# Kernel tuning notes

Measured on AMD Instinct MI355X. Metric: run time of the kernel, lower is better.

## Reference

```python
import jax, jax.numpy as jnp
import numpy as np

N, K, F_IN, T, OUT = 50000, 25, 128, 256, 128
EPS = 1e-3  # TF BatchNormalization default epsilon


def batchnorm_train(x, gamma, beta):
    # training-mode BN: biased batch statistics over axis 0
    mean = jnp.mean(x, axis=0)
    var = jnp.var(x, axis=0)
    return (x - mean) * jax.lax.rsqrt(var + EPS) * gamma + beta


def setup_inputs() -> dict:
    key = jax.random.key(0)
    ks = jax.random.split(key, 6)
    return {
        "self_nodes": jax.random.normal(ks[0], (N, F_IN), dtype=jnp.float32),
        "neigh_nodes": jax.random.normal(ks[1], (N, K, F_IN), dtype=jnp.float32),
        "len_adj_nodes": jax.random.randint(ks[2], (N,), 1, K + 1, dtype=jnp.int32),
        "Wt": jax.random.normal(ks[3], (F_IN, T), dtype=jnp.float32) * 0.05,
        "bt": jnp.zeros((T,), dtype=jnp.float32),
        "g1": jnp.ones((T,), dtype=jnp.float32),
        "b1": jnp.zeros((T,), dtype=jnp.float32),
        "Wn": jax.random.normal(ks[4], (T, OUT), dtype=jnp.float32) * 0.05,
        "Ws": jax.random.normal(ks[5], (F_IN, OUT), dtype=jnp.float32) * 0.05,
        "g2": jnp.ones((2 * OUT,), dtype=jnp.float32),
        "b2": jnp.zeros((2 * OUT,), dtype=jnp.float32),
    }


def reference(self_nodes, neigh_nodes, len_adj_nodes, Wt, bt, g1, b1, Wn, Ws, g2, b2):
    # len_adj_nodes is accepted by the original call() but unused.
    # transform neighbor features: [N, K, F_IN] -> [N, K, T]
    neigh = jnp.einsum('nkf,ft->nkt', neigh_nodes, Wt) + bt
    # bn1 over flattened [N*K, T] (training mode)
    neigh = batchnorm_train(neigh.reshape(-1, T), g1, b1).reshape(N, K, T)
    # pool_op = reduce_max over the neighbor axis
    pooled = jnp.max(neigh, axis=1)            # [N, T]
    neigh_out = pooled @ Wn                     # [N, OUT], no bias
    self_out = self_nodes @ Ws                  # [N, OUT], no bias
    out = jnp.concatenate([self_out, neigh_out], axis=1)  # use_concat=True
    out = batchnorm_train(out, g2, b2)
    return jax.nn.relu(out)
```

## Files before the change

### kernel.cpp

```cpp
#include <hip/hip_runtime.h>


#define NN 50000
#define KN 25
#define FIN 128
#define TD 256
#define OUTD 128
#define BN_EPS 1e-3f
#define NSLOTS 64
#define K1_GRID 512
#define NGROUPS (NN / 2)

typedef float f32x4 __attribute__((ext_vector_type(4)));
typedef short bf16x8 __attribute__((ext_vector_type(8)));

__device__ __forceinline__ ushort f2bf(float f) {
    uint u = __builtin_bit_cast(uint, f);
    return (ushort)((u + 0x7FFFu + ((u >> 16) & 1u)) >> 16);
}
__device__ __forceinline__ uint pk2(float a, float b) {
    return (uint)f2bf(a) | ((uint)f2bf(b) << 16);
}
__device__ __forceinline__ float bflo(uint u) {
    return __builtin_bit_cast(float, u << 16);
}
__device__ __forceinline__ float bfhi(uint u) {
    return __builtin_bit_cast(float, u & 0xffff0000u);
}

__global__ __launch_bounds__(256) void k0_prep(
    const float* __restrict__ Ws, const float* __restrict__ Wn,
    float* __restrict__ stats, ushort* __restrict__ WsT, ushort* __restrict__ WnT)
{
    const int gid = blockIdx.x * 256 + threadIdx.x;
    if (gid < 65536) {
        stats[gid] = 0.f;
    } else if (gid < 81920) {
        const int t = gid - 65536, col = t >> 7, k = t & 127;
        WsT[col * FIN + k] = f2bf(Ws[k * OUTD + col]);
    } else {
        const int t = gid - 81920, col = t >> 8, k = t & 255;
        WnT[col * TD + k] = f2bf(Wn[k * OUTD + col]);
    }
}

__global__ __launch_bounds__(256, 2) void k1_gemm_pool(
    const float* __restrict__ neigh, const float* __restrict__ Wt,
    const float* __restrict__ bt, uint* __restrict__ nmm,
    float* __restrict__ s1sum, float* __restrict__ s1sq)
{
    __shared__ ushort lds[32768];
    const int tid = threadIdx.x;
    const int wave = tid >> 6, lane = tid & 63;
    const int quad = lane >> 4, l16 = lane & 15;
    const int cbase = wave * 64;

    {
        const float4* w4 = (const float4*)Wt;
        #pragma unroll
        for (int i = 0; i < 32; ++i) {
            const int e = tid + i * 256;
            const int k = e >> 6, c4 = (e & 63) << 2;
            const float4 v = w4[e];
            uint* dst = (uint*)&lds[k * 256 + c4];
            dst[0] = pk2(v.x, v.y);
            dst[1] = pk2(v.z, v.w);
        }
    }
    __syncthreads();

    bf16x8 bf[4][4];
    #pragma unroll
    for (int nt = 0; nt < 4; ++nt) {
        const int col = cbase + nt * 16 + l16;
        #pragma unroll
        for (int ks = 0; ks < 4; ++ks) {
            #pragma unroll
            for (int j = 0; j < 8; ++j)
                bf[nt][ks][j] = (short)lds[(ks * 32 + quad * 8 + j) * 256 + col];
        }
    }
    __syncthreads();

    float bv[4];
    #pragma unroll
    for (int n = 0; n < 4; ++n) bv[n] = bt[cbase + n * 16 + l16];

    float S[4] = {0.f, 0.f, 0.f, 0.f}, Q[4] = {0.f, 0.f, 0.f, 0.f};

    int g = blockIdx.x;
    {
        const float4* src = (const float4*)(neigh + (size_t)g * 6400);
        #pragma unroll
        for (int i = 0; i < 7; ++i) {
            const int idx = tid + i * 256;
            if (idx < 1600) {
                const float4 v = src[idx];
                const int r = idx >> 5;
                const int pr = r + (r >= 25 ? 7 : 0);
                uint* dst = (uint*)&lds[pr * 136 + ((idx & 31) << 2)];
                dst[0] = pk2(v.x, v.y);
                dst[1] = pk2(v.z, v.w);
            }
        }
    }
    __syncthreads();

    int cur = 0;
    for (; g < NGROUPS; g += K1_GRID) {
        const int gn = g + K1_GRID;
        float4 pre[7];
        if (gn < NGROUPS) {
            const float4* src = (const float4*)(neigh + (size_t)gn * 6400);
            #pragma unroll
            for (int i = 0; i < 7; ++i) {
                const int idx = tid + i * 256;
                if (idx < 1600) pre[i] = src[idx];
            }
        }
        const ushort* Ab = lds + cur * 8704;
        f32x4 acc[4][4];
        #pragma unroll
        for (int m = 0; m < 4; ++m)
            #pragma unroll
            for (int n = 0; n < 4; ++n)
                acc[m][n] = (f32x4){0.f, 0.f, 0.f, 0.f};
        #pragma unroll
        for (int m = 0; m < 4; ++m) {
            bf16x8 af[4];
            #pragma unroll
            for (int ks = 0; ks < 4; ++ks)
                af[ks] = *(const bf16x8*)&Ab[(m * 16 + l16) * 136 + ks * 32 + quad * 8];
            #pragma unroll
            for (int n = 0; n < 4; ++n)
                #pragma unroll
                for (int ks = 0; ks < 4; ++ks)
                    acc[m][n] = __builtin_amdgcn_mfma_f32_16x16x32_bf16(af[ks], bf[n][ks], acc[m][n], 0, 0, 0);
        }
        #pragma unroll
        for (int gi = 0; gi < 2; ++gi) {
            const int node = g * 2 + gi;
            #pragma unroll
            for (int n = 0; n < 4; ++n) {
                float mx = -3.4e38f, mn = 3.4e38f;
                #pragma unroll
                for (int i = 0; i < 4; ++i) {
                    const float v = acc[2 * gi][n][i] + bv[n];
                    mx = fmaxf(mx, v); mn = fminf(mn, v);
                    S[n] += v; Q[n] = fmaf(v, v, Q[n]);
                }
                #pragma unroll
                for (int i = 0; i < 4; ++i) {
                    if (quad * 4 + i < 9) {
                        const float v = acc[2 * gi + 1][n][i] + bv[n];
                        mx = fmaxf(mx, v); mn = fminf(mn, v);
                        S[n] += v; Q[n] = fmaf(v, v, Q[n]);
                    }
                }
                mx = fmaxf(mx, __shfl_xor(mx, 16)); mx = fmaxf(mx, __shfl_xor(mx, 32));
                mn = fminf(mn, __shfl_xor(mn, 16)); mn = fminf(mn, __shfl_xor(mn, 32));
                if (lane < 16)
                    nmm[node * TD + cbase + n * 16 + lane] = pk2(mx, mn);
            }
        }
        if (gn < NGROUPS) {
            ushort* Aw = lds + (cur ^ 1) * 8704;
            #pragma unroll
            for (int i = 0; i < 7; ++i) {
                const int idx = tid + i * 256;
                if (idx < 1600) {
                    const int r = idx >> 5;
                    const int pr = r + (r >= 25 ? 7 : 0);
                    uint* dst = (uint*)&Aw[pr * 136 + ((idx & 31) << 2)];
                    dst[0] = pk2(pre[i].x, pre[i].y);
                    dst[1] = pk2(pre[i].z, pre[i].w);
                }
            }
        }
        __syncthreads();
        cur ^= 1;
    }
    #pragma unroll
    for (int n = 0; n < 4; ++n) {
        float s = S[n]; s += __shfl_xor(s, 16); s += __shfl_xor(s, 32);
        float q = Q[n]; q += __shfl_xor(q, 16); q += __shfl_xor(q, 32);
        if (lane < 16) {
            const int col = cbase + n * 16 + lane;
            const int slot = blockIdx.x & (NSLOTS - 1);
            atomicAdd(&s1sum[slot * TD + col], s);
            atomicAdd(&s1sq[slot * TD + col], q);
        }
    }
}

__global__ __launch_bounds__(256) void k_stats(
    const float* __restrict__ ssum, const float* __restrict__ ssq,
    const float* __restrict__ g, const float* __restrict__ b,
    float invM, float* __restrict__ a, float* __restrict__ cc)
{
    const int c = threadIdx.x;
    float s = 0.f, q = 0.f;
    for (int j = 0; j < NSLOTS; ++j) { s += ssum[j * TD + c]; q += ssq[j * TD + c]; }
    const float mean = s * invM;
    const float var = q * invM - mean * mean;
    const float A = rsqrtf(var + BN_EPS) * g[c];
    a[c] = A;
    cc[c] = fmaf(-mean, A, b[c]);
}

__global__ __launch_bounds__(256, 2) void k2_gemm2(
    const float* __restrict__ selfn, const uint* __restrict__ nmm,
    const ushort* __restrict__ WsT, const ushort* __restrict__ WnT,
    const float* __restrict__ s1sum, const float* __restrict__ s1sq,
    const float* __restrict__ g1, const float* __restrict__ b1,
    float* __restrict__ Y, float* __restrict__ s2sum, float* __restrict__ s2sq)
{
    __shared__ ushort lds[25600];
    __shared__ float aL[256], cL[256];
    const int tid = threadIdx.x;
    const int wave = tid >> 6, lane = tid & 63;
    const int quad = lane >> 4, l16 = lane & 15;
    const int R0 = blockIdx.x * 64;

    {
        const int c = tid;
        float s = 0.f, q = 0.f;
        #pragma unroll 8
        for (int j = 0; j < NSLOTS; ++j) { s += s1sum[j * TD + c]; q += s1sq[j * TD + c]; }
        const float invM = 1.f / (float)((size_t)NN * KN);
        const float mean = s * invM;
        const float var = q * invM - mean * mean;
        const float A = rsqrtf(var + BN_EPS) * g1[c];
        aL[c] = A;
        cL[c] = fmaf(-mean, A, b1[c]);
    }

    {
        const float4* s4 = (const float4*)selfn;
        #pragma unroll
        for (int i = 0; i < 8; ++i) {
            const int e = tid + i * 256;
            const int r = e >> 5, k4 = e & 31;
            const int gr = R0 + r;
            const float4 v = (gr < NN) ? s4[(size_t)gr * 32 + k4] : make_float4(0.f, 0.f, 0.f, 0.f);
            uint* dst = (uint*)&lds[r * 136 + (k4 << 2)];
            dst[0] = pk2(v.x, v.y);
            dst[1] = pk2(v.z, v.w);
        }
    }
    __syncthreads();

    {
        const uint4* m4 = (const uint4*)nmm;
        #pragma unroll
        for (int i = 0; i < 16; ++i) {
            const int e = tid + i * 256;
            const int r = e >> 6, c4 = e & 63;
            const int gr = R0 + r;
            uint4 v;
            if (gr < NN) v = m4[(size_t)gr * 64 + c4];
            else { v.x = 0u; v.y = 0u; v.z = 0u; v.w = 0u; }
            const float4 a = *(const float4*)&aL[c4 << 2];
            const float4 c = *(const float4*)&cL[c4 << 2];
            const float p0 = (a.x >= 0.f) ? fmaf(a.x, bflo(v.x), c.x) : fmaf(a.x, bfhi(v.x), c.x);
            const float p1 = (a.y >= 0.f) ? fmaf(a.y, bflo(v.y), c.y) : fmaf(a.y, bfhi(v.y), c.y);
            const float p2 = (a.z >= 0.f) ? fmaf(a.z, bflo(v.z), c.z) : fmaf(a.z, bfhi(v.z), c.z);
            const float p3 = (a.w >= 0.f) ? fmaf(a.w, bflo(v.w), c.w) : fmaf(a.w, bfhi(v.w), c.w);
            uint* dst = (uint*)&lds[8704 + r * 264 + (c4 << 2)];
            dst[0] = pk2(p0, p1);
            dst[1] = pk2(p2, p3);
        }
    }
    __syncthreads();

    f32x4 acc[4][4];
    #pragma unroll
    for (int m = 0; m < 4; ++m)
        #pragma unroll
        for (int n = 0; n < 4; ++n)
            acc[m][n] = (f32x4){0.f, 0.f, 0.f, 0.f};

    if (wave < 2) {
        const int cb = wave * 64;
        bf16x8 bfr[4][4];
        #pragma unroll
        for (int nt = 0; nt < 4; ++nt)
            #pragma unroll
            for (int ks = 0; ks < 4; ++ks)
                bfr[nt][ks] = *(const bf16x8*)&WsT[(cb + nt * 16 + l16) * FIN + ks * 32 + quad * 8];
        #pragma unroll
        for (int m = 0; m < 4; ++m) {
            bf16x8 af[4];
            #pragma unroll
            for (int ks = 0; ks < 4; ++ks)
                af[ks] = *(const bf16x8*)&lds[(m * 16 + l16) * 136 + ks * 32 + quad * 8];
            #pragma unroll
            for (int nt = 0; nt < 4; ++nt)
                #pragma unroll
                for (int ks = 0; ks < 4; ++ks)
                    acc[m][nt] = __builtin_amdgcn_mfma_f32_16x16x32_bf16(af[ks], bfr[nt][ks], acc[m][nt], 0, 0, 0);
        }
    } else {
        const int cb = (wave - 2) * 64;
        bf16x8 bfr[4][8];
        #pragma unroll
        for (int nt = 0; nt < 4; ++nt)
            #pragma unroll
            for (int ks = 0; ks < 8; ++ks)
                bfr[nt][ks] = *(const bf16x8*)&WnT[(cb + nt * 16 + l16) * TD + ks * 32 + quad * 8];
        #pragma unroll
        for (int m = 0; m < 4; ++m) {
            bf16x8 af[8];
            #pragma unroll
            for (int ks = 0; ks < 8; ++ks)
                af[ks] = *(const bf16x8*)&lds[8704 + (m * 16 + l16) * 264 + ks * 32 + quad * 8];
            #pragma unroll
            for (int nt = 0; nt < 4; ++nt)
                #pragma unroll
                for (int ks = 0; ks < 8; ++ks)
                    acc[m][nt] = __builtin_amdgcn_mfma_f32_16x16x32_bf16(af[ks], bfr[nt][ks], acc[m][nt], 0, 0, 0);
        }
    }

    const int colb = wave * 64;
    float S[4] = {0.f, 0.f, 0.f, 0.f}, Q[4] = {0.f, 0.f, 0.f, 0.f};
    #pragma unroll
    for (int m = 0; m < 4; ++m) {
        #pragma unroll
        for (int nt = 0; nt < 4; ++nt) {
            #pragma unroll
            for (int i = 0; i < 4; ++i) {
                const int row = R0 + m * 16 + quad * 4 + i;
                const float v = acc[m][nt][i];
                if (row < NN) {
                    Y[(size_t)row * TD + colb + nt * 16 + l16] = v;
                    S[nt] += v;
                    Q[nt] = fmaf(v, v, Q[nt]);
                }
            }
        }
    }
    #pragma unroll
    for (int nt = 0; nt < 4; ++nt) {
        float s = S[nt]; s += __shfl_xor(s, 16); s += __shfl_xor(s, 32);
        float q = Q[nt]; q += __shfl_xor(q, 16); q += __shfl_xor(q, 32);
        if (lane < 16) {
            const int col = colb + nt * 16 + lane;
            const int slot = blockIdx.x & (NSLOTS - 1);
            atomicAdd(&s2sum[slot * TD + col], s);
            atomicAdd(&s2sq[slot * TD + col], q);
        }
    }
}

__global__ __launch_bounds__(256) void k7_bn_relu(
    float* __restrict__ out, const float* __restrict__ a2, const float* __restrict__ c2)
{
    const int idx = blockIdx.x * 256 + threadIdx.x;
    const int c4 = idx & 63;
    float4 y = ((const float4*)out)[idx];
    const float4 a = ((const float4*)a2)[c4];
    const float4 c = ((const float4*)c2)[c4];
    y.x = fmaxf(0.f, fmaf(a.x, y.x, c.x));
    y.y = fmaxf(0.f, fmaf(a.y, y.y, c.y));
    y.z = fmaxf(0.f, fmaf(a.z, y.z, c.z));
    y.w = fmaxf(0.f, fmaf(a.w, y.w, c.w));
    ((float4*)out)[idx] = y;
}

extern "C" void kernel_launch(void* const* d_in, const int* in_sizes, int n_in,
                              void* d_out, int out_size, void* d_ws, size_t ws_size,
                              hipStream_t stream) {
    const float* selfn = (const float*)d_in[0];
    const float* neigh = (const float*)d_in[1];
    const float* Wt = (const float*)d_in[3];
    const float* bt = (const float*)d_in[4];
    const float* g1 = (const float*)d_in[5];
    const float* b1 = (const float*)d_in[6];
    const float* Wn = (const float*)d_in[7];
    const float* Ws = (const float*)d_in[8];
    const float* g2 = (const float*)d_in[9];
    const float* b2 = (const float*)d_in[10];
    float* out = (float*)d_out;

    float* ws = (float*)d_ws;
    uint* nmm = (uint*)ws;
    float* s1sum = ws + (size_t)NN * TD;
    float* s1sq = s1sum + NSLOTS * TD;
    float* s2sum = s1sq + NSLOTS * TD;
    float* s2sq = s2sum + NSLOTS * TD;
    float* a2 = s2sq + NSLOTS * TD;
    float* c2 = a2 + TD;
    ushort* WsT = (ushort*)(c2 + TD);
    ushort* WnT = WsT + FIN * OUTD;

    k0_prep<<<448, 256, 0, stream>>>(Ws, Wn, s1sum, WsT, WnT);
    k1_gemm_pool<<<K1_GRID, 256, 0, stream>>>(neigh, Wt, bt, nmm, s1sum, s1sq);
    k2_gemm2<<<(NN + 63) / 64, 256, 0, stream>>>(selfn, nmm, WsT, WnT, s1sum, s1sq,
                                                 g1, b1, out, s2sum, s2sq);
    k_stats<<<1, 256, 0, stream>>>(s2sum, s2sq, g2, b2, 1.f / (float)NN, a2, c2);
    k7_bn_relu<<<NN * TD / 4 / 256, 256, 0, stream>>>(out, a2, c2);
}
```

Before: 1.049 ms.

## Drop weight prep kernel, compute BN1 stats once, convert weights in-kernel

Removes the k0_prep kernel and replaces the stats zeroing with hipMemsetAsync. Each k2 block now converts Ws/Wn to bf16 directly from global memory with strided scalar loads instead of reading pre-transposed bf16 copies. BN1 scale and shift are computed once by a separate k_stats launch rather than redundantly in every k2 block. The aim is to avoid the per-block 64-slot reduction and one prep kernel, at the cost of uncoalesced weight reads in all ~780 k2 blocks and an extra tiny launch.

Result: no change. 1.046 ms (-0.3%).

```diff
diff --git a/kernel.cpp b/kernel.cpp
--- a/kernel.cpp
+++ b/kernel.cpp
@@ -26,22 +26,6 @@
 }
 __device__ __forceinline__ float bfhi(uint u) {
     return __builtin_bit_cast(float, u & 0xffff0000u);
-}
-
-__global__ __launch_bounds__(256) void k0_prep(
-    const float* __restrict__ Ws, const float* __restrict__ Wn,
-    float* __restrict__ stats, ushort* __restrict__ WsT, ushort* __restrict__ WnT)
-{
-    const int gid = blockIdx.x * 256 + threadIdx.x;
-    if (gid < 65536) {
-        stats[gid] = 0.f;
-    } else if (gid < 81920) {
-        const int t = gid - 65536, col = t >> 7, k = t & 127;
-        WsT[col * FIN + k] = f2bf(Ws[k * OUTD + col]);
-    } else {
-        const int t = gid - 81920, col = t >> 8, k = t & 255;
-        WnT[col * TD + k] = f2bf(Wn[k * OUTD + col]);
-    }
 }
 
 __global__ __launch_bounds__(256, 2) void k1_gemm_pool(
@@ -210,30 +194,15 @@
 
 __global__ __launch_bounds__(256, 2) void k2_gemm2(
     const float* __restrict__ selfn, const uint* __restrict__ nmm,
-    const ushort* __restrict__ WsT, const ushort* __restrict__ WnT,
-    const float* __restrict__ s1sum, const float* __restrict__ s1sq,
-    const float* __restrict__ g1, const float* __restrict__ b1,
+    const float* __restrict__ Ws, const float* __restrict__ Wn,
+    const float* __restrict__ a1, const float* __restrict__ c1,
     float* __restrict__ Y, float* __restrict__ s2sum, float* __restrict__ s2sq)
 {
     __shared__ ushort lds[25600];
-    __shared__ float aL[256], cL[256];
     const int tid = threadIdx.x;
     const int wave = tid >> 6, lane = tid & 63;
     const int quad = lane >> 4, l16 = lane & 15;
     const int R0 = blockIdx.x * 64;
-
-    {
-        const int c = tid;
-        float s = 0.f, q = 0.f;
-        #pragma unroll 8
-        for (int j = 0; j < NSLOTS; ++j) { s += s1sum[j * TD + c]; q += s1sq[j * TD + c]; }
-        const float invM = 1.f / (float)((size_t)NN * KN);
-        const float mean = s * invM;
-        const float var = q * invM - mean * mean;
-        const float A = rsqrtf(var + BN_EPS) * g1[c];
-        aL[c] = A;
-        cL[c] = fmaf(-mean, A, b1[c]);
-    }
 
     {
         const float4* s4 = (const float4*)selfn;
@@ -248,10 +217,10 @@
             dst[1] = pk2(v.z, v.w);
         }
     }
-    __syncthreads();
-
     {
         const uint4* m4 = (const uint4*)nmm;
+        const float4* a4p = (const float4*)a1;
+        const float4* c4p = (const float4*)c1;
         #pragma unroll
         for (int i = 0; i < 16; ++i) {
             const int e = tid + i * 256;
@@ -260,8 +229,7 @@
             uint4 v;
             if (gr < NN) v = m4[(size_t)gr * 64 + c4];
             else { v.x = 0u; v.y = 0u; v.z = 0u; v.w = 0u; }
-            const float4 a = *(const float4*)&aL[c4 << 2];
-            const float4 c = *(const float4*)&cL[c4 << 2];
+            const float4 a = a4p[c4], c = c4p[c4];
             const float p0 = (a.x >= 0.f) ? fmaf(a.x, bflo(v.x), c.x) : fmaf(a.x, bfhi(v.x), c.x);
             const float p1 = (a.y >= 0.f) ? fmaf(a.y, bflo(v.y), c.y) : fmaf(a.y, bfhi(v.y), c.y);
             const float p2 = (a.z >= 0.f) ? fmaf(a.z, bflo(v.z), c.z) : fmaf(a.z, bfhi(v.z), c.z);
@@ -287,7 +255,9 @@
         for (int nt = 0; nt < 4; ++nt)
             #pragma unroll
             for (int ks = 0; ks < 4; ++ks)
-                bfr[nt][ks] = *(const bf16x8*)&WsT[(cb + nt * 16 + l16) * FIN + ks * 32 + quad * 8];
+                #pragma unroll
+                for (int j = 0; j < 8; ++j)
+                    bfr[nt][ks][j] = (short)f2bf(Ws[(ks * 32 + quad * 8 + j) * OUTD + cb + nt * 16 + l16]);
         #pragma unroll
         for (int m = 0; m < 4; ++m) {
             bf16x8 af[4];
@@ -307,7 +277,9 @@
         for (int nt = 0; nt < 4; ++nt)
             #pragma unroll
             for (int ks = 0; ks < 8; ++ks)
-                bfr[nt][ks] = *(const bf16x8*)&WnT[(cb + nt * 16 + l16) * TD + ks * 32 + quad * 8];
+                #pragma unroll
+                for (int j = 0; j < 8; ++j)
+                    bfr[nt][ks][j] = (short)f2bf(Wn[(ks * 32 + quad * 8 + j) * OUTD + cb + nt * 16 + l16]);
         #pragma unroll
         for (int m = 0; m < 4; ++m) {
             bf16x8 af[8];
@@ -389,15 +361,16 @@
     float* s1sq = s1sum + NSLOTS * TD;
     float* s2sum = s1sq + NSLOTS * TD;
     float* s2sq = s2sum + NSLOTS * TD;
-    float* a2 = s2sq + NSLOTS * TD;
+    float* a1 = s2sq + NSLOTS * TD;
+    float* c1 = a1 + TD;
+    float* a2 = c1 + TD;
     float* c2 = a2 + TD;
-    ushort* WsT = (ushort*)(c2 + TD);
-    ushort* WnT = WsT + FIN * OUTD;
-
-    k0_prep<<<448, 256, 0, stream>>>(Ws, Wn, s1sum, WsT, WnT);
+
+    hipMemsetAsync(s1sum, 0, (size_t)4 * NSLOTS * TD * sizeof(float), stream);
+
     k1_gemm_pool<<<K1_GRID, 256, 0, stream>>>(neigh, Wt, bt, nmm, s1sum, s1sq);
-    k2_gemm2<<<(NN + 63) / 64, 256, 0, stream>>>(selfn, nmm, WsT, WnT, s1sum, s1sq,
-                                                 g1, b1, out, s2sum, s2sq);
+    k_stats<<<1, 256, 0, stream>>>(s1sum, s1sq, g1, b1, 1.f / (float)(NN * KN), a1, c1);
+    k2_gemm2<<<(NN + 63) / 64, 256, 0, stream>>>(selfn, nmm, Ws, Wn, a1, c1, out, s2sum, s2sq);
     k_stats<<<1, 256, 0, stream>>>(s2sum, s2sq, g2, b2, 1.f / (float)NN, a2, c2);
     k7_bn_relu<<<NN * TD / 4 / 256, 256, 0, stream>>>(out, a2, c2);
 }
```
